# Optimization experiments

Measured on AMD Instinct MI355X. Metric: run time of the kernel, lower is better.

Reference implementation:

```python
import jax, jax.numpy as jnp
import numpy as np

B, L, S, H, E = 4, 1024, 1024, 8, 64


def setup_inputs() -> dict:
    key = jax.random.key(0)
    ks = jax.random.split(key, 8)
    return {
        "query": jax.random.normal(ks[0], (B, L, H, E), dtype=jnp.float32),
        "key": jax.random.normal(ks[1], (B, S, H, E), dtype=jnp.float32),
        "value": jax.random.normal(ks[2], (B, S, H, E), dtype=jnp.float32),
        "phi": jax.random.normal(ks[3], (H, L, S), dtype=jnp.float32),
        "log_gain": jnp.asarray(np.log(10.0), dtype=jnp.float32),
        "log_tau": jnp.asarray(np.log(2.0), dtype=jnp.float32),
        "log_tau_comm": jnp.asarray(np.log(0.2), dtype=jnp.float32),
        "hard_mask": jax.random.uniform(ks[4], (L, S), dtype=jnp.float32),
        "u": jax.random.uniform(ks[5], (H, L, S), dtype=jnp.float32),
        "mask_miss_k": jnp.ones((B, S), dtype=jnp.float32),
        "mask_miss_q": jnp.ones((B, L), dtype=jnp.float32),
        "pos": jnp.zeros((B, L), dtype=jnp.float32),
        "causal_mask": 0,
    }


def reference(query, key, value, phi, log_gain, log_tau, log_tau_comm,
              hard_mask, u, mask_miss_k, mask_miss_q, pos, causal_mask):
    # mask_miss_k/q, pos, causal_mask are unused by LieAttention.forward (torch parity)
    E_dim = query.shape[-1]
    scale = 1.0 / float(np.sqrt(E_dim))
    # raw scores (B, H, L, S)
    scores = jnp.einsum('blhe,bshe->bhls', query, key)
    # antisymmetric communication term
    comm = scores - jnp.swapaxes(scores, -1, -2)
    gain = jnp.clip(jnp.exp(log_gain), 1e-3, 1000.0)      # max_gain = 1000
    tau_comm = jnp.clip(jnp.exp(log_tau_comm), 1e-3, 10.0)
    comm_amp = jnp.tanh((gain / tau_comm) * comm)
    att = scale * jax.nn.gelu(comm_amp, approximate=False)  # torch F.gelu = exact erf
    # Gumbel-sigmoid relaxed DAG mask, broadcast over batch: M (1, H, L, S)
    tau = jnp.clip(jnp.exp(log_tau), 0.1, 5.0)             # tau_min/tau_max
    m_relaxed = jax.nn.sigmoid((jnp.log(u + 1e-8) - jnp.log(1.0 - u + 1e-8) + phi) / tau)
    att = att * m_relaxed[None]
    # hard mask (L, S) -> (1, 1, L, S)
    att = att * hard_mask[None, None]
    # attention entropy per query position: (B, H, L)
    eps = 1e-8
    entropy = jnp.nan_to_num(-jnp.sum(att * jnp.log(jnp.maximum(att, eps)), axis=-1))
    A = jnp.nan_to_num(att)  # dropout=0.0 -> identity
    V = jnp.einsum('bhls,bshd->blhd', A, value)
    return V, A, entropy
```

## Files before the change

### kernel.cpp

```cpp
#include <hip/hip_runtime.h>
#include <math.h>

#define Bn 4
#define Ln 1024
#define Sn 1024
#define Hn 8
#define En 64

typedef __attribute__((ext_vector_type(4))) float f32x4;
typedef __attribute__((ext_vector_type(8))) _Float16 h16x8;
typedef __attribute__((ext_vector_type(4))) _Float16 h16x4;

__device__ __forceinline__ float frcp(float x) { return __builtin_amdgcn_rcpf(x); }
__device__ __forceinline__ float fexp2(float x) {
    float r; asm("v_exp_f32 %0, %1" : "=v"(r) : "v"(x)); return r;
}
__device__ __forceinline__ float flog2(float x) {
    float r; asm("v_log_f32 %0, %1" : "=v"(r) : "v"(x)); return r;
}

__global__ __launch_bounds__(256) void prep(
    const float* __restrict__ Q, const float* __restrict__ K,
    const float* __restrict__ V,
    _Float16* __restrict__ Qh, _Float16* __restrict__ Ql,
    _Float16* __restrict__ Kh, _Float16* __restrict__ Kl,
    _Float16* __restrict__ Vt, float* __restrict__ Vout,
    float* __restrict__ entOut) {
    __shared__ float vlds[16][69];
    const int bx = blockIdx.x;
    const int st = bx >> 2;
    const int rg = bx & 3;
    const int bh = blockIdx.y;
    const int b = bh >> 3, h = bh & 7;
    const int tid = threadIdx.x;
    const int s0 = st * 64;

    {
        const int flat = (blockIdx.y * 64 + bx) * 256 + tid;
        *(f32x4*)(Vout + (size_t)flat * 4) = (f32x4){0.f, 0.f, 0.f, 0.f};
        if (flat < 8192) *(f32x4*)(entOut + (size_t)flat * 4) = (f32x4){0.f, 0.f, 0.f, 0.f};
    }

    {
        const int r16 = tid >> 4;
        const int c4 = (tid & 15) << 2;
        const int row = rg * 16 + r16;
        size_t gin = (((size_t)b * Ln + s0 + row) * Hn + h) * En + c4;
        f32x4 qv = *(const f32x4*)(Q + gin);
        f32x4 kv = *(const f32x4*)(K + gin);
        f32x4 vv = *(const f32x4*)(V + gin);
        vlds[r16][c4 + 0] = vv.x; vlds[r16][c4 + 1] = vv.y;
        vlds[r16][c4 + 2] = vv.z; vlds[r16][c4 + 3] = vv.w;
        h16x4 qh4, ql4, kh4, kl4;
#pragma unroll
        for (int j = 0; j < 4; ++j) {
            float x = qv[j];
            _Float16 hx = (_Float16)x;
            qh4[j] = hx; ql4[j] = (_Float16)(x - (float)hx);
            float y = kv[j];
            _Float16 hy = (_Float16)y;
            kh4[j] = hy; kl4[j] = (_Float16)(y - (float)hy);
        }
        size_t ob = ((((size_t)bh * 16 + st) * 8 + (c4 >> 3)) * 64 + row) * 8 + (c4 & 7);
        *(h16x4*)(Qh + ob) = qh4; *(h16x4*)(Ql + ob) = ql4;
        *(h16x4*)(Kh + ob) = kh4; *(h16x4*)(Kl + ob) = kl4;
    }
    __syncthreads();
    {
        const int d = tid >> 2;
        const int sgl = (tid & 3) << 2;
        h16x4 v4;
#pragma unroll
        for (int j = 0; j < 4; ++j) v4[j] = (_Float16)vlds[sgl + j][d];
        const int sg = rg * 16 + sgl;
        size_t ob = ((((size_t)bh * 16 + st) * 8 + (sg >> 3)) * 64 + d) * 8 + (sg & 7);
        *(h16x4*)(Vt + ob) = v4;
    }
}

__global__ __launch_bounds__(256) void prep2(
    const float* __restrict__ phi, const float* __restrict__ u,
    const float* __restrict__ hard, const float* __restrict__ p_lt,
    _Float16* __restrict__ mh) {
    const float tau = fminf(fmaxf(expf(p_lt[0]), 0.1f), 5.0f);
    const float itau = 1.0f / tau;
    const size_t base = ((size_t)blockIdx.x * 256 + threadIdx.x) * 8;
    const size_t ls = base & (size_t)(Ln * Sn - 1);
    f32x4 ph0 = *(const f32x4*)(phi + base);
    f32x4 ph1 = *(const f32x4*)(phi + base + 4);
    f32x4 uu0 = *(const f32x4*)(u + base);
    f32x4 uu1 = *(const f32x4*)(u + base + 4);
    f32x4 hm0 = *(const f32x4*)(hard + ls);
    f32x4 hm1 = *(const f32x4*)(hard + ls + 4);
    h16x8 o;
#pragma unroll
    for (int j = 0; j < 4; ++j) {
        float z = (__logf((uu0[j] + 1e-8f) * frcp(1.0f - uu0[j] + 1e-8f)) + ph0[j]) * itau;
        float m = frcp(1.0f + __expf(-z));
        o[j] = (_Float16)(0.125f * m * hm0[j]);
    }
#pragma unroll
    for (int j = 0; j < 4; ++j) {
        float z = (__logf((uu1[j] + 1e-8f) * frcp(1.0f - uu1[j] + 1e-8f)) + ph1[j]) * itau;
        float m = frcp(1.0f + __expf(-z));
        o[4 + j] = (_Float16)(0.125f * m * hm1[j]);
    }
    *(h16x8*)(mh + base) = o;
}

__global__ __launch_bounds__(256, 4) void fused_lie(
    const _Float16* __restrict__ Qh, const _Float16* __restrict__ Ql,
    const _Float16* __restrict__ Kh, const _Float16* __restrict__ Kl,
    const _Float16* __restrict__ Vt, const _Float16* __restrict__ mh,
    const float* __restrict__ p_lg, const float* __restrict__ p_ltc,
    float* __restrict__ Aout, float* __restrict__ Vout,
    float* __restrict__ entOut) {
    __shared__ __align__(16) _Float16 plds[4][16 * 72];

    const int f = blockIdx.x;
    const int work = (f & 7) * 256 + (f >> 3);
    const int h = work >> 8;
    const int rem = work & 255;
    const int b = rem >> 6;
    const int tile = rem & 63;
    const int lt = tile >> 2;
    const int sq = tile & 3;
    const int bh = b * Hn + h;
    const int tid = threadIdx.x;
    const int w = tid >> 6;
    const int lane = tid & 63;
    const int q = lane >> 4;
    const int n = lane & 15;
    const int l0 = lt * 64;

    const float gain = fminf(fmaxf(expf(p_lg[0]), 1e-3f), 1000.0f);
    const float tauc = fminf(fmaxf(expf(p_ltc[0]), 1e-3f), 10.0f);
    const float c2l = 2.0f * gain / tauc * 1.44269504f;

    h16x8 QAh[2], QAl[2], KAh[2], KAl[2];
    {
        const size_t ab = (((size_t)bh * 16 + lt) * 8) * 512 + (size_t)(w * 16 + n) * 8;
#pragma unroll
        for (int kh = 0; kh < 2; ++kh) {
            size_t off = ab + (size_t)(q + 4 * kh) * 512;
            QAh[kh] = *(const h16x8*)(Qh + off);
            QAl[kh] = *(const h16x8*)(Ql + off);
            KAh[kh] = *(const h16x8*)(Kh + off);
            KAl[kh] = *(const h16x8*)(Kl + off);
        }
    }

    f32x4 accV[4];
#pragma unroll
    for (int i = 0; i < 4; ++i) accV[i] = (f32x4){0.f, 0.f, 0.f, 0.f};
    float entp[4] = {0.f, 0.f, 0.f, 0.f};

    const int lbase = l0 + w * 16 + q * 4;
    float* __restrict__ arow = Aout + (((size_t)b * Hn + h) * Ln + lbase) * (size_t)Sn;
    const _Float16* __restrict__ ment = mh + ((size_t)h * Ln + lbase) * (size_t)Sn;

    for (int stc = 0; stc < 4; ++stc) {
        const int st = sq * 4 + stc;
        const int s0 = st * 64;
        const size_t tb = (((size_t)bh * 16 + st) * 8) * 512;

#pragma unroll
        for (int sub = 0; sub < 4; ++sub) {
            f32x4 x1 = (f32x4){0.f, 0.f, 0.f, 0.f};
            f32x4 x2 = (f32x4){0.f, 0.f, 0.f, 0.f};
#pragma unroll
            for (int kh = 0; kh < 2; ++kh) {
                const size_t off = tb + (size_t)(q + 4 * kh) * 512 + (size_t)(sub * 16 + n) * 8;
                h16x8 KBh = *(const h16x8*)(Kh + off);
                h16x8 KBl = *(const h16x8*)(Kl + off);
                h16x8 QBh = *(const h16x8*)(Qh + off);
                h16x8 QBl = *(const h16x8*)(Ql + off);
                x1 = __builtin_amdgcn_mfma_f32_16x16x32_f16(QAh[kh], KBh, x1, 0, 0, 0);
                x1 = __builtin_amdgcn_mfma_f32_16x16x32_f16(QAh[kh], KBl, x1, 0, 0, 0);
                x1 = __builtin_amdgcn_mfma_f32_16x16x32_f16(QAl[kh], KBh, x1, 0, 0, 0);
                x2 = __builtin_amdgcn_mfma_f32_16x16x32_f16(KAh[kh], QBh, x2, 0, 0, 0);
                x2 = __builtin_amdgcn_mfma_f32_16x16x32_f16(KAh[kh], QBl, x2, 0, 0, 0);
                x2 = __builtin_amdgcn_mfma_f32_16x16x32_f16(KAl[kh], QBh, x2, 0, 0, 0);
            }
            const int s = s0 + sub * 16 + n;
#pragma unroll
            for (int r = 0; r < 4; ++r) {
                float mhv = (float)ment[(size_t)r * Sn + s];
                float cm = x1[r] - x2[r];
                float x = 1.0f - 2.0f * frcp(fexp2(c2l * cm) + 1.0f);
                float t = x * fmaf(0.044715f * x, x, 1.0f);
                float g = x * frcp(1.0f + fexp2(-2.30221271f * t));
                float att = g * mhv;
                __builtin_nontemporal_store(att, &arow[(size_t)r * Sn + s]);
                entp[r] += att * flog2(fmaxf(att, 1e-8f));
                plds[w][(q * 4 + r) * 72 + sub * 16 + n] = (_Float16)att;
            }
        }
        asm volatile("" ::: "memory");

        {
            const _Float16* pw = &plds[w][0];
#pragma unroll
            for (int kh = 0; kh < 2; ++kh) {
                const size_t kqb = tb + (size_t)(q + 4 * kh) * 512;
                h16x8 Pf = *(const h16x8*)&pw[n * 72 + q * 8 + kh * 32];
#pragma unroll
                for (int sub = 0; sub < 4; ++sub) {
                    h16x8 Vf = *(const h16x8*)(Vt + kqb + (size_t)(sub * 16 + n) * 8);
                    accV[sub] = __builtin_amdgcn_mfma_f32_16x16x32_f16(Pf, Vf, accV[sub], 0, 0, 0);
                }
            }
        }
        asm volatile("" ::: "memory");
    }

#pragma unroll
    for (int sub = 0; sub < 4; ++sub) {
#pragma unroll
        for (int r = 0; r < 4; ++r) {
            const int l = l0 + w * 16 + q * 4 + r;
            atomicAdd(Vout + (((size_t)b * Ln + l) * Hn + h) * En + sub * 16 + n, accV[sub][r]);
        }
    }
#pragma unroll
    for (int r = 0; r < 4; ++r) {
        float v = entp[r];
        v += __shfl_xor(v, 1);
        v += __shfl_xor(v, 2);
        v += __shfl_xor(v, 4);
        v += __shfl_xor(v, 8);
        if (n == 0) {
            atomicAdd(entOut + ((size_t)b * Hn + h) * Ln + lbase + r, -v * 0.69314718f);
        }
    }
}

extern "C" void kernel_launch(void* const* d_in, const int* in_sizes, int n_in,
                              void* d_out, int out_size, void* d_ws, size_t ws_size,
                              hipStream_t stream) {
    (void)in_sizes; (void)n_in; (void)ws_size; (void)out_size;

    const float* Q    = (const float*)d_in[0];
    const float* K    = (const float*)d_in[1];
    const float* Vv   = (const float*)d_in[2];
    const float* phi  = (const float*)d_in[3];
    const float* lg   = (const float*)d_in[4];
    const float* ltau = (const float*)d_in[5];
    const float* ltc  = (const float*)d_in[6];
    const float* hard = (const float*)d_in[7];
    const float* u    = (const float*)d_in[8];

    float* out  = (float*)d_out;
    float* Vout = out;
    float* Aout = out + (size_t)Bn * Ln * Hn * En;
    float* ent  = Aout + (size_t)Bn * Hn * Ln * Sn;

    const size_t NE = (size_t)32 * 1024 * 64;
    _Float16* Qh = (_Float16*)d_ws;
    _Float16* Ql = Qh + NE;
    _Float16* Kh = Ql + NE;
    _Float16* Kl = Kh + NE;
    _Float16* Vt = Kl + NE;
    _Float16* mh = Vt + NE;

    prep<<<dim3(64, 32), 256, 0, stream>>>(Q, K, Vv, Qh, Ql, Kh, Kl, Vt, Vout, ent);
    prep2<<<dim3(4096), 256, 0, stream>>>(phi, u, hard, ltau, mh);
    fused_lie<<<dim3(2048), 256, 0, stream>>>(Qh, Ql, Kh, Kl, Vt, mh,
                                              lg, ltc, Aout, Vout, ent);
}
```

Measured before the change: 389.7 us.

## Halve grid, batch score MFMAs per tile and prefetch V fragments early

```diff
diff --git a/kernel.cpp b/kernel.cpp
--- a/kernel.cpp
+++ b/kernel.cpp
@@ -118,13 +118,13 @@
     __shared__ __align__(16) _Float16 plds[4][16 * 72];
 
     const int f = blockIdx.x;
-    const int work = (f & 7) * 256 + (f >> 3);
-    const int h = work >> 8;
-    const int rem = work & 255;
-    const int b = rem >> 6;
-    const int tile = rem & 63;
-    const int lt = tile >> 2;
-    const int sq = tile & 3;
+    const int work = (f & 7) * 128 + (f >> 3);
+    const int h = work >> 7;
+    const int rem = work & 127;
+    const int b = rem >> 5;
+    const int tile = rem & 31;
+    const int lt = tile >> 1;
+    const int sh = tile & 1;
     const int bh = b * Hn + h;
     const int tid = threadIdx.x;
     const int w = tid >> 6;
@@ -159,34 +159,54 @@
     float* __restrict__ arow = Aout + (((size_t)b * Hn + h) * Ln + lbase) * (size_t)Sn;
     const _Float16* __restrict__ ment = mh + ((size_t)h * Ln + lbase) * (size_t)Sn;
 
-    for (int stc = 0; stc < 4; ++stc) {
-        const int st = sq * 4 + stc;
+    for (int stc = 0; stc < 8; ++stc) {
+        const int st = sh * 8 + stc;
         const int s0 = st * 64;
         const size_t tb = (((size_t)bh * 16 + st) * 8) * 512;
 
-#pragma unroll
-        for (int sub = 0; sub < 4; ++sub) {
-            f32x4 x1 = (f32x4){0.f, 0.f, 0.f, 0.f};
-            f32x4 x2 = (f32x4){0.f, 0.f, 0.f, 0.f};
-#pragma unroll
-            for (int kh = 0; kh < 2; ++kh) {
-                const size_t off = tb + (size_t)(q + 4 * kh) * 512 + (size_t)(sub * 16 + n) * 8;
+        h16x8 Vf[2][4];
+#pragma unroll
+        for (int kh = 0; kh < 2; ++kh) {
+            const size_t kqb = tb + (size_t)(q + 4 * kh) * 512;
+#pragma unroll
+            for (int sub = 0; sub < 4; ++sub)
+                Vf[kh][sub] = *(const h16x8*)(Vt + kqb + (size_t)(sub * 16 + n) * 8);
+        }
+
+        f32x4 a1[4], a2[4];
+#pragma unroll
+        for (int i = 0; i < 4; ++i) {
+            a1[i] = (f32x4){0.f, 0.f, 0.f, 0.f};
+            a2[i] = (f32x4){0.f, 0.f, 0.f, 0.f};
+        }
+#pragma unroll
+        for (int kh = 0; kh < 2; ++kh) {
+            const size_t kqb = tb + (size_t)(q + 4 * kh) * 512;
+#pragma unroll
+            for (int sub = 0; sub < 4; ++sub) {
+                const size_t off = kqb + (size_t)(sub * 16 + n) * 8;
                 h16x8 KBh = *(const h16x8*)(Kh + off);
                 h16x8 KBl = *(const h16x8*)(Kl + off);
                 h16x8 QBh = *(const h16x8*)(Qh + off);
                 h16x8 QBl = *(const h16x8*)(Ql + off);
+                f32x4 x1 = a1[sub], x2 = a2[sub];
                 x1 = __builtin_amdgcn_mfma_f32_16x16x32_f16(QAh[kh], KBh, x1, 0, 0, 0);
                 x1 = __builtin_amdgcn_mfma_f32_16x16x32_f16(QAh[kh], KBl, x1, 0, 0, 0);
                 x1 = __builtin_amdgcn_mfma_f32_16x16x32_f16(QAl[kh], KBh, x1, 0, 0, 0);
                 x2 = __builtin_amdgcn_mfma_f32_16x16x32_f16(KAh[kh], QBh, x2, 0, 0, 0);
                 x2 = __builtin_amdgcn_mfma_f32_16x16x32_f16(KAh[kh], QBl, x2, 0, 0, 0);
                 x2 = __builtin_amdgcn_mfma_f32_16x16x32_f16(KAl[kh], QBh, x2, 0, 0, 0);
+                a1[sub] = x1; a2[sub] = x2;
             }
+        }
+
+#pragma unroll
+        for (int sub = 0; sub < 4; ++sub) {
             const int s = s0 + sub * 16 + n;
 #pragma unroll
             for (int r = 0; r < 4; ++r) {
                 float mhv = (float)ment[(size_t)r * Sn + s];
-                float cm = x1[r] - x2[r];
+                float cm = a1[sub][r] - a2[sub][r];
                 float x = 1.0f - 2.0f * frcp(fexp2(c2l * cm) + 1.0f);
                 float t = x * fmaf(0.044715f * x, x, 1.0f);
                 float g = x * frcp(1.0f + fexp2(-2.30221271f * t));
@@ -196,22 +216,18 @@
                 plds[w][(q * 4 + r) * 72 + sub * 16 + n] = (_Float16)att;
             }
         }
-        asm volatile("" ::: "memory");
 
         {
             const _Float16* pw = &plds[w][0];
 #pragma unroll
             for (int kh = 0; kh < 2; ++kh) {
-                const size_t kqb = tb + (size_t)(q + 4 * kh) * 512;
                 h16x8 Pf = *(const h16x8*)&pw[n * 72 + q * 8 + kh * 32];
 #pragma unroll
                 for (int sub = 0; sub < 4; ++sub) {
-                    h16x8 Vf = *(const h16x8*)(Vt + kqb + (size_t)(sub * 16 + n) * 8);
-                    accV[sub] = __builtin_amdgcn_mfma_f32_16x16x32_f16(Pf, Vf, accV[sub], 0, 0, 0);
+                    accV[sub] = __builtin_amdgcn_mfma_f32_16x16x32_f16(Pf, Vf[kh][sub], accV[sub], 0, 0, 0);
                 }
             }
         }
-        asm volatile("" ::: "memory");
     }
 
 #pragma unroll
@@ -265,6 +281,6 @@
 
     prep<<<dim3(64, 32), 256, 0, stream>>>(Q, K, Vv, Qh, Ql, Kh, Kl, Vt, Vout, ent);
     prep2<<<dim3(4096), 256, 0, stream>>>(phi, u, hard, ltau, mh);
-    fused_lie<<<dim3(2048), 256, 0, stream>>>(Qh, Ql, Kh, Kl, Vt, mh,
+    fused_lie<<<dim3(1024), 256, 0, stream>>>(Qh, Ql, Kh, Kl, Vt, mh,
                                               lg, ltc, Aout, Vout, ent);
 }
```

Result: faster. 373.2 us (-4.2%).
